# Optimization experiments

Measured on AMD Instinct MI355X. Metric: run time of the kernel, lower is better.

Reference implementation:

```python
import jax, jax.numpy as jnp
import numpy as np

ALPHA = 0.2        # LeakyReLU negative slope
NEG_BIG = -9e15    # mask fill value from the original module


def setup_inputs() -> dict:
    key = jax.random.key(0)
    k1, k2, k3, k4 = jax.random.split(key, 4)
    B, N, F_in, F_out = 4, 4096, 128, 64
    h = jax.random.normal(k1, (B, N, F_in), dtype=jnp.float32)
    adj = jax.random.randint(k2, (N, N), 0, 2, dtype=jnp.int32)
    W = jax.random.normal(k3, (F_in, F_out), dtype=jnp.float32)
    a = jax.random.normal(k4, (2 * F_out, 1), dtype=jnp.float32)
    return {"h": h, "adj": adj, "W": W, "a": a}


def reference(h, adj, W, a):
    # h: [B, N, F_in], adj: [N, N], W: [F_in, F_out], a: [2*F_out, 1]
    F_out = W.shape[1]
    hW = jnp.einsum('bni,io->bno', h, W)               # [B, N, F_out]
    f1 = hW @ a[:F_out, :]                             # [B, N, 1]
    f2 = hW @ a[F_out:, :]                             # [B, N, 1]
    e = f1 + jnp.swapaxes(f2, 1, 2)                    # [B, N, N] broadcast-add
    e = jax.nn.leaky_relu(e, negative_slope=ALPHA)
    e = jax.nn.softmax(e, axis=2)
    # dropout is a no-op (is_training=False)
    attention = jnp.where(adj[None, :, :] > 0, e, NEG_BIG)
    new_h = jax.nn.sigmoid(jnp.einsum('bnm,bmo->bno', attention, hW))
    return new_h
```

## Files before the change

### kernel.cpp

```cpp
#include <hip/hip_runtime.h>
#include <hip/hip_bf16.h>


#define GN 4096
#define GB 4
#define FIN 128
#define FOUT 64
#define FLAG_CAP 65536

typedef int i32x4 __attribute__((ext_vector_type(4)));
typedef unsigned int uint32x4 __attribute__((ext_vector_type(4)));
typedef float f32x4 __attribute__((ext_vector_type(4)));

__global__ __launch_bounds__(256) void pack_kernel(const int* __restrict__ adj,
                                                   unsigned long long* __restrict__ tmask,
                                                   unsigned int* __restrict__ counter) {
    if (blockIdx.x == 0 && threadIdx.x == 0) *counter = 0;
    int wid = blockIdx.x * 4 + (threadIdx.x >> 6);
    int lane = threadIdx.x & 63;
    int rt = wid >> 6, s = wid & 63;
    int row16 = lane & 15, g = lane >> 4;
    const int* base = adj + (size_t)(rt * 64 + row16) * GN + s * 64 + g * 16;
    unsigned long long res = 0ull;
#pragma unroll
    for (int r = 0; r < 4; ++r) {
        const i32x4* p = (const i32x4*)(base + (size_t)r * 16 * GN);
        unsigned int b16 = 0;
#pragma unroll
        for (int q = 0; q < 4; ++q) {
            i32x4 v = p[q];
            b16 |= (v.x == 0 ? 1u : 0u) << (q * 4);
            b16 |= (v.y == 0 ? 2u : 0u) << (q * 4);
            b16 |= (v.z == 0 ? 4u : 0u) << (q * 4);
            b16 |= (v.w == 0 ? 8u : 0u) << (q * 4);
        }
        res |= (unsigned long long)b16 << (r * 16);
    }
    tmask[(size_t)wid * 64 + lane] = res;
}

__global__ __launch_bounds__(256) void hw_kernel(const float* __restrict__ h,
                                                 const float* __restrict__ W,
                                                 double* __restrict__ hW) {
    const int grp = threadIdx.x >> 6;
    const int o = threadIdx.x & 63;
    const int bn = blockIdx.x * 4 + grp;
    __shared__ float hs[4][FIN];
    {
        const f32x4* src = (const f32x4*)(h + (size_t)blockIdx.x * 4 * FIN);
        f32x4* dst = (f32x4*)&hs[0][0];
        if (threadIdx.x < 128) dst[threadIdx.x] = src[threadIdx.x];
    }
    __syncthreads();
    double a0 = 0, a1 = 0, a2 = 0, a3 = 0;
#pragma unroll
    for (int i = 0; i < FIN; i += 4) {
        a0 = fma((double)hs[grp][i],     (double)W[i * FOUT + o],       a0);
        a1 = fma((double)hs[grp][i + 1], (double)W[(i + 1) * FOUT + o], a1);
        a2 = fma((double)hs[grp][i + 2], (double)W[(i + 2) * FOUT + o], a2);
        a3 = fma((double)hs[grp][i + 3], (double)W[(i + 3) * FOUT + o], a3);
    }
    double acc = (a0 + a1) + (a2 + a3);
    hW[(size_t)bn * FOUT + o] = acc;
}

__global__ __launch_bounds__(256) void repack_kernel(const double* __restrict__ hW,
                                                     unsigned char* __restrict__ Bp) {
    const int b = blockIdx.x >> 6, p = blockIdx.x & 63;
    const int t = threadIdx.x;
    const int cg = t >> 6, g = (t >> 4) & 3, col16 = t & 15;
    const int o = cg * 16 + col16;
    const double* src = hW + ((size_t)b * GN + p * 64 + g * 16) * FOUT + o;
    uint32x4 w0 = {0, 0, 0, 0}, w1 = {0, 0, 0, 0}, w2 = {0, 0, 0, 0};
#pragma unroll
    for (int jj = 0; jj < 16; ++jj) {
        double v = src[(size_t)jj * FOUT];
        int qi = (int)llrint(v * 65536.0);
        int d0 = ((qi + 128) & 255) - 128; qi = (qi - d0) >> 8;
        int d1 = ((qi + 128) & 255) - 128; qi = (qi - d1) >> 8;
        int wi = jj >> 2, sh = (jj & 3) * 8;
        w0[wi] |= (unsigned int)(d0 & 255) << sh;
        w1[wi] |= (unsigned int)(d1 & 255) << sh;
        w2[wi] |= (unsigned int)(qi & 255) << sh;
    }
    unsigned char* dst = Bp + (size_t)blockIdx.x * 12288 + (size_t)cg * 1024 + g * 256 + col16 * 16;
    *(uint32x4*)(dst) = w0;
    *(uint32x4*)(dst + 4096) = w1;
    *(uint32x4*)(dst + 8192) = w2;
}

__global__ __launch_bounds__(512, 1) void gemm_kernel(const unsigned char* __restrict__ Bp,
                                                      const unsigned long long* __restrict__ tmask,
                                                      float* __restrict__ out,
                                                      unsigned int* __restrict__ flags,
                                                      unsigned int* __restrict__ counter) {
    __shared__ __align__(16) unsigned char lds[4 * 24576 + 32768];
    unsigned long long* tml = (unsigned long long*)(lds + 4 * 24576);

    const int tid = threadIdx.x, lane = tid & 63, wv = tid >> 6;
    const int cg = wv & 3, kg = wv >> 2;
    const int rt = (int)blockIdx.x >> 2, b = (int)blockIdx.x & 3;

    const unsigned char* bpb = Bp + (size_t)b * (64 * 12288);
    const unsigned char* tmg = (const unsigned char*)(tmask + (size_t)rt * 4096);

#pragma unroll
    for (int q = 0; q < 4; ++q)
        __builtin_amdgcn_global_load_lds((const unsigned int*)(tmg + q * 8192 + tid * 16),
                                         (unsigned int*)(lds + 4 * 24576 + q * 8192 + tid * 16), 16, 0, 0);
#pragma unroll
    for (int t0 = 0; t0 < 3; ++t0)
#pragma unroll
        for (int seg = 0; seg < 3; ++seg)
            __builtin_amdgcn_global_load_lds(
                (const unsigned int*)(bpb + (size_t)t0 * 24576 + seg * 8192 + tid * 16),
                (unsigned int*)(lds + t0 * 24576 + seg * 8192 + tid * 16), 16, 0, 0);
    __syncthreads();

    i32x4 acc[4][3];
#pragma unroll
    for (int r = 0; r < 4; ++r)
#pragma unroll
        for (int pl = 0; pl < 3; ++pl) {
            i32x4 z = {0, 0, 0, 0};
            acc[r][pl] = z;
        }

    const int boff = cg * 1024 + lane * 16;

#define GSTEP(T, VM, DO_ISSUE)                                                          \
    {                                                                                   \
        asm volatile("s_waitcnt vmcnt(" #VM ")" ::: "memory");                          \
        __builtin_amdgcn_s_barrier();                                                   \
        const unsigned char* buf = lds + ((T) & 3) * 24576 + kg * 12288;                \
        i32x4 b0 = *(const i32x4*)(buf + boff);                                         \
        i32x4 b1 = *(const i32x4*)(buf + boff + 4096);                                  \
        i32x4 b2 = *(const i32x4*)(buf + boff + 8192);                                  \
        unsigned long long mw = tml[(size_t)(2 * (T) + kg) * 64 + lane];                \
        if (DO_ISSUE) {                                                                 \
            const unsigned char* gsrc = bpb + (size_t)((T) + 3) * 24576;                \
            unsigned char* gdst = lds + (((T) + 3) & 3) * 24576;                        \
            _Pragma("unroll")                                                           \
            for (int seg = 0; seg < 3; ++seg)                                           \
                __builtin_amdgcn_global_load_lds(                                       \
                    (const unsigned int*)(gsrc + seg * 8192 + tid * 16),                \
                    (unsigned int*)(gdst + seg * 8192 + tid * 16), 16, 0, 0);           \
        }                                                                               \
        const unsigned int mlo = (unsigned int)mw, mhi = (unsigned int)(mw >> 32);      \
        i32x4 afr[4];                                                                   \
        _Pragma("unroll")                                                               \
        for (int r = 0; r < 4; ++r) {                                                   \
            unsigned int half = (r >> 1) ? mhi : mlo;                                   \
            unsigned int w16 = (r & 1) ? (half >> 16) : (half & 0xFFFFu);               \
            uint32x4 u;                                                                 \
            _Pragma("unroll")                                                           \
            for (int q = 0; q < 4; ++q)                                                 \
                u[q] = (((w16 >> (4 * q)) & 0xFu) * 0x00204081u) & 0x01010101u;         \
            afr[r] = __builtin_bit_cast(i32x4, u);                                      \
        }                                                                               \
        _Pragma("unroll")                                                               \
        for (int r = 0; r < 4; ++r) {                                                   \
            acc[r][0] = __builtin_amdgcn_mfma_i32_16x16x64_i8(afr[r], b0, acc[r][0], 0, 0, 0); \
            acc[r][1] = __builtin_amdgcn_mfma_i32_16x16x64_i8(afr[r], b1, acc[r][1], 0, 0, 0); \
            acc[r][2] = __builtin_amdgcn_mfma_i32_16x16x64_i8(afr[r], b2, acc[r][2], 0, 0, 0); \
        }                                                                               \
    }

    for (int t = 0; t < 29; ++t) GSTEP(t, 6, 1)
    GSTEP(29, 6, 0)
    GSTEP(30, 3, 0)
    GSTEP(31, 0, 0)
#undef GSTEP

    __syncthreads();
    if (kg == 1) {
        unsigned char* dst = lds + cg * 12288 + lane * 192;
#pragma unroll
        for (int r = 0; r < 4; ++r)
#pragma unroll
            for (int pl = 0; pl < 3; ++pl)
                *(i32x4*)(dst + (r * 3 + pl) * 16) = acc[r][pl];
    }
    __syncthreads();
    if (kg == 0) {
        const unsigned char* s2 = lds + cg * 12288 + lane * 192;
#pragma unroll
        for (int r = 0; r < 4; ++r)
#pragma unroll
            for (int pl = 0; pl < 3; ++pl) {
                i32x4 v = *(const i32x4*)(s2 + (r * 3 + pl) * 16);
#pragma unroll
                for (int q = 0; q < 4; ++q) acc[r][pl][q] += v[q];
            }

        const int o = cg * 16 + (lane & 15);
#pragma unroll
        for (int r = 0; r < 4; ++r) {
#pragma unroll
            for (int q = 0; q < 4; ++q) {
                double S = (double)acc[r][0][q] + 256.0 * (double)acc[r][1][q]
                         + 65536.0 * (double)acc[r][2][q];
                int i = rt * 64 + r * 16 + (lane >> 4) * 4 + q;
                size_t oi = ((size_t)b * GN + i) * FOUT + o;
                out[oi] = S < 0.0 ? 1.0f : 0.0f;
                if (fabs(S) <= 2048.0) {
                    unsigned int idx = atomicAdd(counter, 1u);
                    if (idx < FLAG_CAP) flags[idx] = (unsigned int)oi;
                }
            }
        }
    }
}

__global__ __launch_bounds__(256) void fixup_kernel(const int* __restrict__ adj,
                                                    const double* __restrict__ hW,
                                                    const unsigned int* __restrict__ counter,
                                                    const unsigned int* __restrict__ flags,
                                                    float* __restrict__ out) {
    __shared__ double red[4];
    unsigned int cnt = *counter;
    if (cnt > FLAG_CAP) cnt = FLAG_CAP;
    for (unsigned int f = blockIdx.x; f < cnt; f += gridDim.x) {
        unsigned int e = flags[f];
        int o = e & 63;
        int i = (e >> 6) & 4095;
        int b = (int)(e >> 18);
        double s = 0.0;
#pragma unroll
        for (int it = 0; it < 16; ++it) {
            int j = it * 256 + threadIdx.x;
            int av = adj[(size_t)i * GN + j];
            double v = hW[((size_t)b * GN + j) * FOUT + o];
            s += (av == 0) ? v : 0.0;
        }
#pragma unroll
        for (int d = 32; d >= 1; d >>= 1) s += __shfl_down(s, d, 64);
        if ((threadIdx.x & 63) == 0) red[threadIdx.x >> 6] = s;
        __syncthreads();
        if (threadIdx.x == 0) {
            double tot = (red[0] + red[1]) + (red[2] + red[3]);
            out[e] = tot < 0.0 ? 1.0f : 0.0f;
        }
        __syncthreads();
    }
}

extern "C" void kernel_launch(void* const* d_in, const int* in_sizes, int n_in,
                              void* d_out, int out_size, void* d_ws, size_t ws_size,
                              hipStream_t stream) {
    const float* h   = (const float*)d_in[0];
    const int*   adj = (const int*)d_in[1];
    const float* W   = (const float*)d_in[2];
    float* out = (float*)d_out;

    char* ws = (char*)d_ws;
    double* hW                = (double*)ws;
    unsigned char* Bp         = (unsigned char*)(ws + 8388608);
    unsigned long long* tmask = (unsigned long long*)(ws + 12582912);
    unsigned int* counter     = (unsigned int*)(ws + 16777216);
    unsigned int* flags       = (unsigned int*)(ws + 16777472);

    pack_kernel<<<1024, 256, 0, stream>>>(adj, tmask, counter);
    hw_kernel<<<4096, 256, 0, stream>>>(h, W, hW);
    repack_kernel<<<256, 256, 0, stream>>>(hW, Bp);
    gemm_kernel<<<256, 512, 0, stream>>>(Bp, tmask, out, flags, counter);
    fixup_kernel<<<64, 256, 0, stream>>>(adj, hW, counter, flags, out);
}
```

Measured before the change: 67.41 us.

## Fuse hW and repack kernels; load GEMM operands directly to registers

Merges the hW projection and the int8 digit repack into one kernel. The quantized digits are exchanged through shared memory and written straight to the packed B layout, which removes a launch and the re-read of hW. The GEMM kernel drops its LDS ring buffer and per-step barriers and instead double-buffers B fragments and mask words in registers loaded from global memory. The fixup grid is also doubled. The risks are exposed global load latency without deep prefetch, and small scattered 4-byte stores in the repack.

Measured after the change: 67.57 us. No clear change (+0.2%).

```diff
diff --git a/kernel.cpp b/kernel.cpp
--- a/kernel.cpp
+++ b/kernel.cpp
@@ -39,15 +39,17 @@
     tmask[(size_t)wid * 64 + lane] = res;
 }
 
-__global__ __launch_bounds__(256) void hw_kernel(const float* __restrict__ h,
-                                                 const float* __restrict__ W,
-                                                 double* __restrict__ hW) {
+__global__ __launch_bounds__(256) void hwrepack_kernel(const float* __restrict__ h,
+                                                       const float* __restrict__ W,
+                                                       double* __restrict__ hW,
+                                                       unsigned char* __restrict__ Bp) {
     const int grp = threadIdx.x >> 6;
     const int o = threadIdx.x & 63;
-    const int bn = blockIdx.x * 4 + grp;
+    const int b = blockIdx.x >> 10, q4 = blockIdx.x & 1023;
     __shared__ float hs[4][FIN];
+    __shared__ unsigned int dg[4][64];
     {
-        const f32x4* src = (const f32x4*)(h + (size_t)blockIdx.x * 4 * FIN);
+        const f32x4* src = (const f32x4*)(h + ((size_t)b * GN + q4 * 4) * FIN);
         f32x4* dst = (f32x4*)&hs[0][0];
         if (threadIdx.x < 128) dst[threadIdx.x] = src[threadIdx.x];
     }
@@ -61,32 +63,24 @@
         a3 = fma((double)hs[grp][i + 3], (double)W[(i + 3) * FOUT + o], a3);
     }
     double acc = (a0 + a1) + (a2 + a3);
-    hW[(size_t)bn * FOUT + o] = acc;
-}
-
-__global__ __launch_bounds__(256) void repack_kernel(const double* __restrict__ hW,
-                                                     unsigned char* __restrict__ Bp) {
-    const int b = blockIdx.x >> 6, p = blockIdx.x & 63;
-    const int t = threadIdx.x;
-    const int cg = t >> 6, g = (t >> 4) & 3, col16 = t & 15;
-    const int o = cg * 16 + col16;
-    const double* src = hW + ((size_t)b * GN + p * 64 + g * 16) * FOUT + o;
-    uint32x4 w0 = {0, 0, 0, 0}, w1 = {0, 0, 0, 0}, w2 = {0, 0, 0, 0};
-#pragma unroll
-    for (int jj = 0; jj < 16; ++jj) {
-        double v = src[(size_t)jj * FOUT];
-        int qi = (int)llrint(v * 65536.0);
-        int d0 = ((qi + 128) & 255) - 128; qi = (qi - d0) >> 8;
-        int d1 = ((qi + 128) & 255) - 128; qi = (qi - d1) >> 8;
-        int wi = jj >> 2, sh = (jj & 3) * 8;
-        w0[wi] |= (unsigned int)(d0 & 255) << sh;
-        w1[wi] |= (unsigned int)(d1 & 255) << sh;
-        w2[wi] |= (unsigned int)(qi & 255) << sh;
-    }
-    unsigned char* dst = Bp + (size_t)blockIdx.x * 12288 + (size_t)cg * 1024 + g * 256 + col16 * 16;
-    *(uint32x4*)(dst) = w0;
-    *(uint32x4*)(dst + 4096) = w1;
-    *(uint32x4*)(dst + 8192) = w2;
+    hW[((size_t)b * GN + q4 * 4 + grp) * FOUT + o] = acc;
+
+    int qi = (int)llrint(acc * 65536.0);
+    int d0 = ((qi + 128) & 255) - 128; qi = (qi - d0) >> 8;
+    int d1 = ((qi + 128) & 255) - 128; qi = (qi - d1) >> 8;
+    dg[grp][o] = (unsigned int)(d0 & 255) | ((unsigned int)(d1 & 255) << 8)
+               | ((unsigned int)(qi & 255) << 16);
+    __syncthreads();
+    if (grp < 3) {
+        unsigned int w = 0;
+#pragma unroll
+        for (int rr = 0; rr < 4; ++rr)
+            w |= ((dg[rr][o] >> (grp * 8)) & 255u) << (rr * 8);
+        const int p = q4 >> 4, g = (q4 >> 2) & 3, qr = q4 & 3;
+        const int cg = o >> 4, col16 = o & 15;
+        *(unsigned int*)(Bp + ((size_t)b * 64 + p) * 12288 + grp * 4096
+                         + cg * 1024 + g * 256 + col16 * 16 + qr * 4) = w;
+    }
 }
 
 __global__ __launch_bounds__(512, 1) void gemm_kernel(const unsigned char* __restrict__ Bp,
@@ -94,28 +88,13 @@
                                                       float* __restrict__ out,
                                                       unsigned int* __restrict__ flags,
                                                       unsigned int* __restrict__ counter) {
-    __shared__ __align__(16) unsigned char lds[4 * 24576 + 32768];
-    unsigned long long* tml = (unsigned long long*)(lds + 4 * 24576);
-
+    __shared__ __align__(16) unsigned char lds[49152];
     const int tid = threadIdx.x, lane = tid & 63, wv = tid >> 6;
     const int cg = wv & 3, kg = wv >> 2;
     const int rt = (int)blockIdx.x >> 2, b = (int)blockIdx.x & 3;
 
-    const unsigned char* bpb = Bp + (size_t)b * (64 * 12288);
-    const unsigned char* tmg = (const unsigned char*)(tmask + (size_t)rt * 4096);
-
-#pragma unroll
-    for (int q = 0; q < 4; ++q)
-        __builtin_amdgcn_global_load_lds((const unsigned int*)(tmg + q * 8192 + tid * 16),
-                                         (unsigned int*)(lds + 4 * 24576 + q * 8192 + tid * 16), 16, 0, 0);
-#pragma unroll
-    for (int t0 = 0; t0 < 3; ++t0)
-#pragma unroll
-        for (int seg = 0; seg < 3; ++seg)
-            __builtin_amdgcn_global_load_lds(
-                (const unsigned int*)(bpb + (size_t)t0 * 24576 + seg * 8192 + tid * 16),
-                (unsigned int*)(lds + t0 * 24576 + seg * 8192 + tid * 16), 16, 0, 0);
-    __syncthreads();
+    const unsigned char* bptr = Bp + (size_t)b * 786432 + kg * 12288 + cg * 1024 + lane * 16;
+    const unsigned long long* mptr = tmask + (size_t)rt * 4096 + kg * 64 + lane;
 
     i32x4 acc[4][3];
 #pragma unroll
@@ -126,51 +105,50 @@
             acc[r][pl] = z;
         }
 
-    const int boff = cg * 1024 + lane * 16;
-
-#define GSTEP(T, VM, DO_ISSUE)                                                          \
-    {                                                                                   \
-        asm volatile("s_waitcnt vmcnt(" #VM ")" ::: "memory");                          \
-        __builtin_amdgcn_s_barrier();                                                   \
-        const unsigned char* buf = lds + ((T) & 3) * 24576 + kg * 12288;                \
-        i32x4 b0 = *(const i32x4*)(buf + boff);                                         \
-        i32x4 b1 = *(const i32x4*)(buf + boff + 4096);                                  \
-        i32x4 b2 = *(const i32x4*)(buf + boff + 8192);                                  \
-        unsigned long long mw = tml[(size_t)(2 * (T) + kg) * 64 + lane];                \
-        if (DO_ISSUE) {                                                                 \
-            const unsigned char* gsrc = bpb + (size_t)((T) + 3) * 24576;                \
-            unsigned char* gdst = lds + (((T) + 3) & 3) * 24576;                        \
-            _Pragma("unroll")                                                           \
-            for (int seg = 0; seg < 3; ++seg)                                           \
-                __builtin_amdgcn_global_load_lds(                                       \
-                    (const unsigned int*)(gsrc + seg * 8192 + tid * 16),                \
-                    (unsigned int*)(gdst + seg * 8192 + tid * 16), 16, 0, 0);           \
-        }                                                                               \
-        const unsigned int mlo = (unsigned int)mw, mhi = (unsigned int)(mw >> 32);      \
-        i32x4 afr[4];                                                                   \
-        _Pragma("unroll")                                                               \
-        for (int r = 0; r < 4; ++r) {                                                   \
-            unsigned int half = (r >> 1) ? mhi : mlo;                                   \
-            unsigned int w16 = (r & 1) ? (half >> 16) : (half & 0xFFFFu);               \
-            uint32x4 u;                                                                 \
-            _Pragma("unroll")                                                           \
-            for (int q = 0; q < 4; ++q)                                                 \
-                u[q] = (((w16 >> (4 * q)) & 0xFu) * 0x00204081u) & 0x01010101u;         \
-            afr[r] = __builtin_bit_cast(i32x4, u);                                      \
-        }                                                                               \
-        _Pragma("unroll")                                                               \
-        for (int r = 0; r < 4; ++r) {                                                   \
-            acc[r][0] = __builtin_amdgcn_mfma_i32_16x16x64_i8(afr[r], b0, acc[r][0], 0, 0, 0); \
-            acc[r][1] = __builtin_amdgcn_mfma_i32_16x16x64_i8(afr[r], b1, acc[r][1], 0, 0, 0); \
-            acc[r][2] = __builtin_amdgcn_mfma_i32_16x16x64_i8(afr[r], b2, acc[r][2], 0, 0, 0); \
-        }                                                                               \
-    }
-
-    for (int t = 0; t < 29; ++t) GSTEP(t, 6, 1)
-    GSTEP(29, 6, 0)
-    GSTEP(30, 3, 0)
-    GSTEP(31, 0, 0)
-#undef GSTEP
+    i32x4 ba0 = *(const i32x4*)(bptr);
+    i32x4 ba1 = *(const i32x4*)(bptr + 4096);
+    i32x4 ba2 = *(const i32x4*)(bptr + 8192);
+    unsigned long long ma = mptr[0];
+    i32x4 bb0 = *(const i32x4*)(bptr + 24576);
+    i32x4 bb1 = *(const i32x4*)(bptr + 24576 + 4096);
+    i32x4 bb2 = *(const i32x4*)(bptr + 24576 + 8192);
+    unsigned long long mb = mptr[128];
+
+    auto dostep = [&](unsigned long long mw, i32x4 v0, i32x4 v1, i32x4 v2) {
+        const unsigned int mlo = (unsigned int)mw, mhi = (unsigned int)(mw >> 32);
+#pragma unroll
+        for (int r = 0; r < 4; ++r) {
+            unsigned int half = (r >> 1) ? mhi : mlo;
+            unsigned int w16 = (r & 1) ? (half >> 16) : (half & 0xFFFFu);
+            uint32x4 u;
+#pragma unroll
+            for (int q = 0; q < 4; ++q)
+                u[q] = (((w16 >> (4 * q)) & 0xFu) * 0x00204081u) & 0x01010101u;
+            i32x4 af = __builtin_bit_cast(i32x4, u);
+            acc[r][0] = __builtin_amdgcn_mfma_i32_16x16x64_i8(af, v0, acc[r][0], 0, 0, 0);
+            acc[r][1] = __builtin_amdgcn_mfma_i32_16x16x64_i8(af, v1, acc[r][1], 0, 0, 0);
+            acc[r][2] = __builtin_amdgcn_mfma_i32_16x16x64_i8(af, v2, acc[r][2], 0, 0, 0);
+        }
+    };
+
+    for (int T = 0; T < 32; T += 2) {
+        dostep(ma, ba0, ba1, ba2);
+        if (T + 2 < 32) {
+            const unsigned char* g2 = bptr + (size_t)(T + 2) * 24576;
+            ba0 = *(const i32x4*)(g2);
+            ba1 = *(const i32x4*)(g2 + 4096);
+            ba2 = *(const i32x4*)(g2 + 8192);
+            ma = mptr[(size_t)(T + 2) * 128];
+        }
+        dostep(mb, bb0, bb1, bb2);
+        if (T + 3 < 32) {
+            const unsigned char* g3 = bptr + (size_t)(T + 3) * 24576;
+            bb0 = *(const i32x4*)(g3);
+            bb1 = *(const i32x4*)(g3 + 4096);
+            bb2 = *(const i32x4*)(g3 + 8192);
+            mb = mptr[(size_t)(T + 3) * 128];
+        }
+    }
 
     __syncthreads();
     if (kg == 1) {
@@ -261,8 +239,7 @@
     unsigned int* flags       = (unsigned int*)(ws + 16777472);
 
     pack_kernel<<<1024, 256, 0, stream>>>(adj, tmask, counter);
-    hw_kernel<<<4096, 256, 0, stream>>>(h, W, hW);
-    repack_kernel<<<256, 256, 0, stream>>>(hW, Bp);
+    hwrepack_kernel<<<4096, 256, 0, stream>>>(h, W, hW, Bp);
     gemm_kernel<<<256, 512, 0, stream>>>(Bp, tmask, out, flags, counter);
-    fixup_kernel<<<64, 256, 0, stream>>>(adj, hW, counter, flags, out);
-}
+    fixup_kernel<<<128, 256, 0, stream>>>(adj, hW, counter, flags, out);
+}
```
